# Kernel optimization log

Hardware: AMD Instinct MI355X
Metric: run time of the kernel (lower is better)

Reference implementation:

```python
import jax, jax.numpy as jnp
import numpy as np

N_NODES = 50000
N_EDGES = 800000
IN_DIM = 256
NHID = 64
OUT_DIM = 64
DEPTH = 4
P = 2.0


def _gcn_conv(x, W, b, src, dst, n):
    # PyG GCNConv: xW, add self-loops, sym-normalize, aggregate src->dst, + bias
    xw = x @ W
    loop = jnp.arange(n)
    s = jnp.concatenate([src, loop])
    d = jnp.concatenate([dst, loop])
    deg = jax.ops.segment_sum(jnp.ones_like(d, dtype=xw.dtype), d, num_segments=n)
    dis = jnp.where(deg > 0, jax.lax.rsqrt(jnp.maximum(deg, 1.0)), 0.0)
    w = dis[s] * dis[d]  # [E+n]
    out = jax.ops.segment_sum(w[:, None] * xw[s], d, num_segments=n)
    return out + b


def _g2_gate(x, W, b, src, dst, n):
    xg = jax.nn.relu(_gcn_conv(x, W, b, src, dst, n))
    diff = jnp.abs(xg[src] - xg[dst]) ** P  # [E, nhid]
    sums = jax.ops.segment_sum(diff, src, num_segments=n)
    cnt = jax.ops.segment_sum(jnp.ones((src.shape[0],), dtype=x.dtype), src, num_segments=n)
    return jnp.tanh(sums / jnp.maximum(cnt, 1.0)[:, None])


def setup_inputs() -> dict:
    key = jax.random.key(0)
    ks = jax.random.split(key, 10)
    x = jax.random.normal(ks[0], (N_NODES, IN_DIM), dtype=jnp.float32)
    edge_index = jax.random.randint(ks[1], (2, N_EDGES), 0, N_NODES, dtype=jnp.int64 if jax.config.jax_enable_x64 else jnp.int32)
    s = 0.05
    return {
        "x": x,
        "edge_index": edge_index,
        "enc_w": jax.random.normal(ks[2], (IN_DIM, NHID), dtype=jnp.float32) * s,
        "enc_b": jnp.zeros((NHID,), dtype=jnp.float32),
        "conv_w": jax.random.normal(ks[3], (NHID, NHID), dtype=jnp.float32) * s,
        "conv_b": jnp.zeros((NHID,), dtype=jnp.float32),
        "gg_w": jax.random.normal(ks[4], (NHID, NHID), dtype=jnp.float32) * s,
        "gg_b": jnp.zeros((NHID,), dtype=jnp.float32),
        "dec_w": jax.random.normal(ks[5], (NHID, OUT_DIM), dtype=jnp.float32) * s,
        "dec_b": jnp.zeros((OUT_DIM,), dtype=jnp.float32),
    }


def reference(x, edge_index, enc_w, enc_b, conv_w, conv_b, gg_w, gg_b, dec_w, dec_b):
    n = x.shape[0]
    src, dst = edge_index[0], edge_index[1]
    # eval mode: dropouts are identity
    X = jax.nn.relu(x @ enc_w + enc_b)
    for _ in range(DEPTH):
        X_ = jax.nn.relu(_gcn_conv(X, conv_w, conv_b, src, dst, n))
        tau = _g2_gate(X, gg_w, gg_b, src, dst, n)
        X = (1.0 - tau) * X + tau * X_
    X = jax.nn.relu(X @ dec_w + dec_b)
    return X
```

## Files before the change

kernel.cpp:

```cpp
#include <hip/hip_runtime.h>
#include <math.h>

#define NN 50000
#define NE 800000
#define IND 256
#define NH 64
#define DEPTH 4
#define PART_DIV 6250


__device__ __forceinline__ unsigned short f2bf(float f) {
    unsigned int x = __float_as_uint(f);
    unsigned int r = (x + 0x7fffu + ((x >> 16) & 1u)) >> 16;
    return (unsigned short)r;
}
__device__ __forceinline__ unsigned int pack2bf(float lo, float hi) {
    return (unsigned int)f2bf(lo) | ((unsigned int)f2bf(hi) << 16);
}
__device__ __forceinline__ ushort4 f4_to_us4(float4 f) {
    ushort4 u;
    u.x = f2bf(f.x); u.y = f2bf(f.y); u.z = f2bf(f.z); u.w = f2bf(f.w);
    return u;
}
__device__ __forceinline__ void acc8(float* a, uint4 r) {
    a[0] += __uint_as_float(r.x << 16); a[1] += __uint_as_float(r.x & 0xffff0000u);
    a[2] += __uint_as_float(r.y << 16); a[3] += __uint_as_float(r.y & 0xffff0000u);
    a[4] += __uint_as_float(r.z << 16); a[5] += __uint_as_float(r.z & 0xffff0000u);
    a[6] += __uint_as_float(r.w << 16); a[7] += __uint_as_float(r.w & 0xffff0000u);
}
__device__ __forceinline__ void unpack8(float* a, uint4 r) {
    a[0] = __uint_as_float(r.x << 16); a[1] = __uint_as_float(r.x & 0xffff0000u);
    a[2] = __uint_as_float(r.y << 16); a[3] = __uint_as_float(r.y & 0xffff0000u);
    a[4] = __uint_as_float(r.z << 16); a[5] = __uint_as_float(r.z & 0xffff0000u);
    a[6] = __uint_as_float(r.w << 16); a[7] = __uint_as_float(r.w & 0xffff0000u);
}
__device__ __forceinline__ void accd8(float* a, const float* xg, uint4 r) {
    float e;
    e = xg[0] - __uint_as_float(r.x << 16);         a[0] += e * e;
    e = xg[1] - __uint_as_float(r.x & 0xffff0000u); a[1] += e * e;
    e = xg[2] - __uint_as_float(r.y << 16);         a[2] += e * e;
    e = xg[3] - __uint_as_float(r.y & 0xffff0000u); a[3] += e * e;
    e = xg[4] - __uint_as_float(r.z << 16);         a[4] += e * e;
    e = xg[5] - __uint_as_float(r.z & 0xffff0000u); a[5] += e * e;
    e = xg[6] - __uint_as_float(r.w << 16);         a[6] += e * e;
    e = xg[7] - __uint_as_float(r.w & 0xffff0000u); a[7] += e * e;
}
__device__ __forceinline__ float tanh_pos(float x) {
    float t = __expf(-2.f * x);
    return (1.f - t) / (1.f + t);
}


__global__ void count_deg(const int* __restrict__ src, const int* __restrict__ dst,
                          int* __restrict__ degin, int* __restrict__ degout) {
    int e = blockIdx.x * blockDim.x + threadIdx.x;
    if (e < NE) {
        atomicAdd(&degout[src[e]], 1);
        atomicAdd(&degin[dst[e]], 1);
    }
}

__global__ void scan2(const int* __restrict__ in0, int* __restrict__ out0,
                      const int* __restrict__ in1, int* __restrict__ out1, int n) {
    __shared__ int sums[1024];
    const int* in = blockIdx.x ? in1 : in0;
    int* out = blockIdx.x ? out1 : out0;
    int t = threadIdx.x;
    int chunk = (n + 1023) / 1024;
    int lo = t * chunk;
    int hi = lo + chunk; if (hi > n) hi = n;
    int s = 0;
    for (int i = lo; i < hi; ++i) s += in[i];
    sums[t] = s;
    __syncthreads();
    for (int off = 1; off < 1024; off <<= 1) {
        int v = (t >= off) ? sums[t - off] : 0;
        __syncthreads();
        sums[t] += v;
        __syncthreads();
    }
    int run = (t == 0) ? 0 : sums[t - 1];
    for (int i = lo; i < hi; ++i) { out[i] = run; run += in[i]; }
    if (t == 0) out[n] = sums[1023];
}

__global__ void init_node(const int* __restrict__ degin, const int* __restrict__ degout,
                          const int* __restrict__ off_dst, const int* __restrict__ off_src,
                          int* __restrict__ cur_dst, int* __restrict__ cur_src,
                          float* __restrict__ dis, float* __restrict__ cntf) {
    int i = blockIdx.x * blockDim.x + threadIdx.x;
    if (i < NN) {
        dis[i] = rsqrtf((float)(degin[i] + 1));
        int od = degout[i];
        cntf[i] = (float)(od > 0 ? od : 1);
        cur_dst[i] = off_dst[i];
        cur_src[i] = off_src[i];
    }
}

__global__ void fill_csr_part(const int* __restrict__ src, const int* __restrict__ dst,
                              int* __restrict__ cur_dst, int* __restrict__ cur_src,
                              int* __restrict__ srcs_by_dst, int* __restrict__ dsts_by_src,
                              int nGroups) {
    int p = blockIdx.x & 7;
    int g = blockIdx.x >> 3;
    for (int e = g * 256 + threadIdx.x; e < NE; e += nGroups * 256) {
        int s = src[e], d = dst[e];
        if (d / PART_DIV == p) {
            int pos = atomicAdd(&cur_dst[d], 1);
            srcs_by_dst[pos] = s;
        }
        if (s / PART_DIV == p) {
            int pos = atomicAdd(&cur_src[s], 1);
            dsts_by_src[pos] = d;
        }
    }
}

template<int K, bool RELU, bool WSC>
__global__ __launch_bounds__(256) void gemm64b(const float* __restrict__ X,
                                               const float* __restrict__ W,
                                               const float* __restrict__ bias,
                                               const float* __restrict__ rowscale,
                                               float* __restrict__ out,
                                               unsigned short* __restrict__ xsc, int n) {
    __shared__ float Ws[64 * 64];
    __shared__ float Xs[64][68];
    int tid = threadIdx.x;
    int row0 = blockIdx.x * 64;
    int r16 = tid >> 4;
    int cg = tid & 15;
    float4 acc[4];
#pragma unroll
    for (int t = 0; t < 4; ++t) acc[t] = make_float4(0.f, 0.f, 0.f, 0.f);

    for (int kc = 0; kc < K; kc += 64) {
        const float4* W4 = (const float4*)(W + (size_t)kc * 64);
        float4* Ws4 = (float4*)Ws;
#pragma unroll
        for (int t = 0; t < 4; ++t) Ws4[tid + t * 256] = W4[tid + t * 256];
#pragma unroll
        for (int t = 0; t < 4; ++t) {
            int r = r16 + t * 16;
            int grow = row0 + r;
            float4 xv = make_float4(0.f, 0.f, 0.f, 0.f);
            if (grow < n) xv = *(const float4*)(X + (size_t)grow * K + kc + cg * 4);
            Xs[r][cg * 4 + 0] = xv.x; Xs[r][cg * 4 + 1] = xv.y;
            Xs[r][cg * 4 + 2] = xv.z; Xs[r][cg * 4 + 3] = xv.w;
        }
        __syncthreads();
#pragma unroll
        for (int k = 0; k < 64; ++k) {
            float4 w4 = ((const float4*)Ws)[k * 16 + cg];
#pragma unroll
            for (int t = 0; t < 4; ++t) {
                float xv = Xs[r16 + t * 16][k];
                acc[t].x += xv * w4.x; acc[t].y += xv * w4.y;
                acc[t].z += xv * w4.z; acc[t].w += xv * w4.w;
            }
        }
        __syncthreads();
    }

    float4 b4 = ((const float4*)bias)[cg];
#pragma unroll
    for (int t = 0; t < 4; ++t) {
        int row = row0 + r16 + t * 16;
        if (row < n) {
            float4 o;
            o.x = acc[t].x + b4.x; o.y = acc[t].y + b4.y;
            o.z = acc[t].z + b4.z; o.w = acc[t].w + b4.w;
            if (RELU) {
                o.x = fmaxf(o.x, 0.f); o.y = fmaxf(o.y, 0.f);
                o.z = fmaxf(o.z, 0.f); o.w = fmaxf(o.w, 0.f);
            }
            ((float4*)(out + (size_t)row * 64))[cg] = o;
            if (WSC) {
                float s = rowscale[row];
                float4 o2 = make_float4(o.x * s, o.y * s, o.z * s, o.w * s);
                ((ushort4*)(xsc + (size_t)row * 64))[cg] = f4_to_us4(o2);
            }
        }
    }
}

template<bool OUTBF>
__global__ __launch_bounds__(256) void gemm64z(const float* __restrict__ Z,
                                               const float* __restrict__ W,
                                               const float* __restrict__ bias,
                                               float* __restrict__ outf,
                                               unsigned short* __restrict__ outb, int n) {
    __shared__ float Ws[64 * 64];
    __shared__ float Xs[64][68];
    int tid = threadIdx.x;
    int row0 = blockIdx.x * 64;
    int r16 = tid >> 4;
    int cg = tid & 15;
    float4 acc[4];
#pragma unroll
    for (int t = 0; t < 4; ++t) acc[t] = make_float4(0.f, 0.f, 0.f, 0.f);

    {
        const float4* W4 = (const float4*)W;
        float4* Ws4 = (float4*)Ws;
#pragma unroll
        for (int t = 0; t < 4; ++t) Ws4[tid + t * 256] = W4[tid + t * 256];
#pragma unroll
        for (int t = 0; t < 4; ++t) {
            int r = r16 + t * 16;
            int grow = row0 + r;
            float4 xv = make_float4(0.f, 0.f, 0.f, 0.f);
            if (grow < n) xv = *(const float4*)(Z + (size_t)grow * 64 + cg * 4);
            Xs[r][cg * 4 + 0] = xv.x; Xs[r][cg * 4 + 1] = xv.y;
            Xs[r][cg * 4 + 2] = xv.z; Xs[r][cg * 4 + 3] = xv.w;
        }
        __syncthreads();
#pragma unroll
        for (int k = 0; k < 64; ++k) {
            float4 w4 = ((const float4*)Ws)[k * 16 + cg];
#pragma unroll
            for (int t = 0; t < 4; ++t) {
                float xv = Xs[r16 + t * 16][k];
                acc[t].x += xv * w4.x; acc[t].y += xv * w4.y;
                acc[t].z += xv * w4.z; acc[t].w += xv * w4.w;
            }
        }
    }

    float4 b4 = ((const float4*)bias)[cg];
#pragma unroll
    for (int t = 0; t < 4; ++t) {
        int row = row0 + r16 + t * 16;
        if (row < n) {
            float4 o;
            o.x = fmaxf(acc[t].x + b4.x, 0.f); o.y = fmaxf(acc[t].y + b4.y, 0.f);
            o.z = fmaxf(acc[t].z + b4.z, 0.f); o.w = fmaxf(acc[t].w + b4.w, 0.f);
            if (OUTBF) {
                ((ushort4*)(outb + (size_t)row * 64))[cg] = f4_to_us4(o);
            } else {
                ((float4*)(outf + (size_t)row * 64))[cg] = o;
            }
        }
    }
}

__global__ __launch_bounds__(256) void zgather(
    const unsigned short* __restrict__ Xbf,
    const int* __restrict__ off, const int* __restrict__ nbr,
    const float* __restrict__ dis, float* __restrict__ Z)
{
    int t = blockIdx.x * 256 + threadIdx.x;
    int node = t >> 3, l8 = t & 7;
    if (node >= NN) return;
    const uint4* Xb = (const uint4*)Xbf;
    float a[8];
    unpack8(a, Xb[(size_t)node * 8 + l8]);
    int lo = off[node], hi = off[node + 1];
    int j = lo;
    for (; j + 3 < hi; j += 4) {
        int s0 = nbr[j], s1 = nbr[j + 1], s2 = nbr[j + 2], s3 = nbr[j + 3];
        uint4 r0 = Xb[(size_t)s0 * 8 + l8];
        uint4 r1 = Xb[(size_t)s1 * 8 + l8];
        uint4 r2 = Xb[(size_t)s2 * 8 + l8];
        uint4 r3 = Xb[(size_t)s3 * 8 + l8];
        acc8(a, r0); acc8(a, r1); acc8(a, r2); acc8(a, r3);
    }
    for (; j < hi; ++j) {
        acc8(a, Xb[(size_t)nbr[j] * 8 + l8]);
    }
    float di = dis[node];
    float* zp = Z + (size_t)node * 64 + l8 * 8;
    *(float4*)(zp)     = make_float4(di * a[0], di * a[1], di * a[2], di * a[3]);
    *(float4*)(zp + 4) = make_float4(di * a[4], di * a[5], di * a[6], di * a[7]);
}

__global__ __launch_bounds__(256) void gate_update8(
    const unsigned short* __restrict__ Cbf, const float* __restrict__ Xn,
    float* __restrict__ X, unsigned short* __restrict__ Xbf,
    const int* __restrict__ off, const int* __restrict__ nbr,
    const float* __restrict__ cntf, const float* __restrict__ dis)
{
    int t = blockIdx.x * 256 + threadIdx.x;
    int node = t >> 3, l8 = t & 7;
    if (node >= NN) return;
    const uint4* Cb = (const uint4*)Cbf;
    float xg[8];
    unpack8(xg, Cb[(size_t)node * 8 + l8]);
    float a[8] = {0.f, 0.f, 0.f, 0.f, 0.f, 0.f, 0.f, 0.f};
    int lo = off[node], hi = off[node + 1];
    int j = lo;
    for (; j + 3 < hi; j += 4) {
        int d0 = nbr[j], d1 = nbr[j + 1], d2 = nbr[j + 2], d3 = nbr[j + 3];
        uint4 r0 = Cb[(size_t)d0 * 8 + l8];
        uint4 r1 = Cb[(size_t)d1 * 8 + l8];
        uint4 r2 = Cb[(size_t)d2 * 8 + l8];
        uint4 r3 = Cb[(size_t)d3 * 8 + l8];
        accd8(a, xg, r0); accd8(a, xg, r1); accd8(a, xg, r2); accd8(a, xg, r3);
    }
    for (; j < hi; ++j) {
        accd8(a, xg, Cb[(size_t)nbr[j] * 8 + l8]);
    }
    float inv = 1.f / cntf[node];
    float di = dis[node];
    const float* xop = X + (size_t)node * 64 + l8 * 8;
    const float* xnp = Xn + (size_t)node * 64 + l8 * 8;
    float o[8];
#pragma unroll
    for (int k = 0; k < 8; ++k) {
        float tau = tanh_pos(a[k] * inv);
        float xo = xop[k], xn = xnp[k];
        o[k] = xo + tau * (xn - xo);
    }
    float* xp = X + (size_t)node * 64 + l8 * 8;
    *(float4*)(xp)     = make_float4(o[0], o[1], o[2], o[3]);
    *(float4*)(xp + 4) = make_float4(o[4], o[5], o[6], o[7]);
    uint4 pk;
    pk.x = pack2bf(o[0] * di, o[1] * di);
    pk.y = pack2bf(o[2] * di, o[3] * di);
    pk.z = pack2bf(o[4] * di, o[5] * di);
    pk.w = pack2bf(o[6] * di, o[7] * di);
    ((uint4*)Xbf)[(size_t)node * 8 + l8] = pk;
}


extern "C" void kernel_launch(void* const* d_in, const int* in_sizes, int n_in,
                              void* d_out, int out_size, void* d_ws, size_t ws_size,
                              hipStream_t stream) {
    const float* x      = (const float*)d_in[0];
    const int*   ei     = (const int*)d_in[1];
    const float* enc_w  = (const float*)d_in[2];
    const float* enc_b  = (const float*)d_in[3];
    const float* conv_w = (const float*)d_in[4];
    const float* conv_b = (const float*)d_in[5];
    const float* gg_w   = (const float*)d_in[6];
    const float* gg_b   = (const float*)d_in[7];
    const float* dec_w  = (const float*)d_in[8];
    const float* dec_b  = (const float*)d_in[9];
    float* out = (float*)d_out;

    const int* src = ei;
    const int* dst = ei + NE;

    char* p = (char*)d_ws;
    auto alloc = [&](size_t bytes) -> void* {
        void* r = (void*)p;
        p += (bytes + 255) & ~(size_t)255;
        return r;
    };
    float* X   = (float*)alloc((size_t)NN * 64 * 4);
    float* Zb  = (float*)alloc((size_t)NN * 64 * 4);
    float* B   = (float*)alloc((size_t)NN * 64 * 4);
    unsigned short* Xbf = (unsigned short*)alloc((size_t)NN * 64 * 2);
    unsigned short* Cbf = (unsigned short*)alloc((size_t)NN * 64 * 2);
    float* dis  = (float*)alloc((size_t)NN * 4);
    float* cntf = (float*)alloc((size_t)NN * 4);
    int* degin   = (int*)alloc((size_t)NN * 4);
    int* degout  = (int*)alloc((size_t)NN * 4);
    int* off_dst = (int*)alloc((size_t)(NN + 1) * 4);
    int* off_src = (int*)alloc((size_t)(NN + 1) * 4);
    int* cur_dst = (int*)alloc((size_t)NN * 4);
    int* cur_src = (int*)alloc((size_t)NN * 4);
    int* sbd     = (int*)alloc((size_t)NE * 4);
    int* dbs     = (int*)alloc((size_t)NE * 4);

    hipMemsetAsync(degin, 0, (size_t)NN * 4, stream);
    hipMemsetAsync(degout, 0, (size_t)NN * 4, stream);

    const int EB = (NE + 255) / 256;
    const int NB = (NN + 255) / 256;
    count_deg<<<EB, 256, 0, stream>>>(src, dst, degin, degout);
    scan2<<<2, 1024, 0, stream>>>(degin, off_dst, degout, off_src, NN);
    init_node<<<NB, 256, 0, stream>>>(degin, degout, off_dst, off_src,
                                      cur_dst, cur_src, dis, cntf);
    const int NGROUPS = 104;
    fill_csr_part<<<8 * NGROUPS, 256, 0, stream>>>(src, dst, cur_dst, cur_src,
                                                   sbd, dbs, NGROUPS);

    const int GB = (NN + 63) / 64;
    const int OB = ((NN * 8) + 255) / 256;

    gemm64b<IND, true, true><<<GB, 256, 0, stream>>>(x, enc_w, enc_b, dis, X, Xbf, NN);

    for (int l = 0; l < DEPTH; ++l) {
        zgather<<<OB, 256, 0, stream>>>(Xbf, off_dst, sbd, dis, Zb);
        gemm64z<false><<<GB, 256, 0, stream>>>(Zb, conv_w, conv_b, B, nullptr, NN);
        gemm64z<true><<<GB, 256, 0, stream>>>(Zb, gg_w, gg_b, nullptr, Cbf, NN);
        gate_update8<<<OB, 256, 0, stream>>>(Cbf, B, X, Xbf, off_src, dbs, cntf, dis);
    }

    gemm64b<NH, true, false><<<GB, 256, 0, stream>>>(X, dec_w, dec_b, nullptr, out, nullptr, NN);
}
```

Measured before the change: 764.7 us.

## Parallelize degree scan across blocks and partition degree counting by node range

Replaces the single-block-per-array 1024-thread serial-chunk scan with a three-phase multi-block scan (wave shuffles, per-block sums, add-back), so the prefix sum uses many CUs instead of two. Degree counting now uses a partitioned grid where each of 8 block groups only performs atomics for nodes in its range, the same scheme fill_csr_part already uses, to keep atomics local. The cost is two extra launches, a temporary buffer, and every partition group re-reading the full edge list.

```diff
diff --git a/kernel.cpp b/kernel.cpp
--- a/kernel.cpp
+++ b/kernel.cpp
@@ -7,6 +7,7 @@
 #define NH 64
 #define DEPTH 4
 #define PART_DIV 6250
+#define SB 49
 
 
 __device__ __forceinline__ unsigned short f2bf(float f) {
@@ -51,37 +52,83 @@
 }
 
 
-__global__ void count_deg(const int* __restrict__ src, const int* __restrict__ dst,
-                          int* __restrict__ degin, int* __restrict__ degout) {
-    int e = blockIdx.x * blockDim.x + threadIdx.x;
-    if (e < NE) {
-        atomicAdd(&degout[src[e]], 1);
-        atomicAdd(&degin[dst[e]], 1);
-    }
-}
-
-__global__ void scan2(const int* __restrict__ in0, int* __restrict__ out0,
-                      const int* __restrict__ in1, int* __restrict__ out1, int n) {
-    __shared__ int sums[1024];
-    const int* in = blockIdx.x ? in1 : in0;
-    int* out = blockIdx.x ? out1 : out0;
+__global__ void count_deg_part(const int* __restrict__ src, const int* __restrict__ dst,
+                               int* __restrict__ degin, int* __restrict__ degout,
+                               int nGroups) {
+    int p = blockIdx.x & 7;
+    int g = blockIdx.x >> 3;
+    for (int e = g * 256 + threadIdx.x; e < NE; e += nGroups * 256) {
+        int s = src[e], d = dst[e];
+        if (d / PART_DIV == p) atomicAdd(&degin[d], 1);
+        if (s / PART_DIV == p) atomicAdd(&degout[s], 1);
+    }
+}
+
+__global__ __launch_bounds__(512) void scan_p1(const int* __restrict__ in0,
+                                               const int* __restrict__ in1,
+                                               int* __restrict__ tmp,
+                                               int* __restrict__ bsum) {
+    int a = blockIdx.x / SB;
+    int b = blockIdx.x % SB;
+    const int* in = a ? in1 : in0;
     int t = threadIdx.x;
-    int chunk = (n + 1023) / 1024;
-    int lo = t * chunk;
-    int hi = lo + chunk; if (hi > n) hi = n;
-    int s = 0;
-    for (int i = lo; i < hi; ++i) s += in[i];
-    sums[t] = s;
+    int base = b * 1024 + t * 2;
+    int v0 = (base < NN) ? in[base] : 0;
+    int v1 = (base + 1 < NN) ? in[base + 1] : 0;
+    int v = v0 + v1;
+    int x = v;
+#pragma unroll
+    for (int off = 1; off < 64; off <<= 1) {
+        int u = __shfl_up(x, off);
+        if ((t & 63) >= off) x += u;
+    }
+    __shared__ int ws[8];
+    int wid = t >> 6, lane = t & 63;
+    if (lane == 63) ws[wid] = x;
     __syncthreads();
-    for (int off = 1; off < 1024; off <<= 1) {
-        int v = (t >= off) ? sums[t - off] : 0;
-        __syncthreads();
-        sums[t] += v;
-        __syncthreads();
-    }
-    int run = (t == 0) ? 0 : sums[t - 1];
-    for (int i = lo; i < hi; ++i) { out[i] = run; run += in[i]; }
-    if (t == 0) out[n] = sums[1023];
+    if (t == 0) {
+        int run = 0;
+#pragma unroll
+        for (int w = 0; w < 8; ++w) { int s = ws[w]; ws[w] = run; run += s; }
+    }
+    __syncthreads();
+    x += ws[wid];
+    int excl = x - v;
+    if (base < NN) tmp[a * NN + base] = excl;
+    if (base + 1 < NN) tmp[a * NN + base + 1] = excl + v0;
+    if (t == 511) bsum[a * SB + b] = x;
+}
+
+__global__ __launch_bounds__(128) void scan_p2(int* __restrict__ bsum,
+                                               int* __restrict__ out0,
+                                               int* __restrict__ out1) {
+    int t = threadIdx.x;
+    int a = t >> 6, lane = t & 63;
+    int v = (lane < SB) ? bsum[a * SB + lane] : 0;
+    int x = v;
+#pragma unroll
+    for (int off = 1; off < 64; off <<= 1) {
+        int u = __shfl_up(x, off);
+        if (lane >= off) x += u;
+    }
+    if (lane < SB) bsum[a * SB + lane] = x - v;
+    if (lane == SB - 1) {
+        if (a == 0) out0[NN] = x; else out1[NN] = x;
+    }
+}
+
+__global__ __launch_bounds__(512) void scan_p3(const int* __restrict__ tmp,
+                                               const int* __restrict__ bsum,
+                                               int* __restrict__ out0,
+                                               int* __restrict__ out1) {
+    int a = blockIdx.x / SB;
+    int b = blockIdx.x % SB;
+    int* out = a ? out1 : out0;
+    int add = bsum[a * SB + b];
+    int t = threadIdx.x;
+    int base = b * 1024 + t * 2;
+    if (base < NN) out[base] = tmp[a * NN + base] + add;
+    if (base + 1 < NN) out[base + 1] = tmp[a * NN + base + 1] + add;
 }
 
 __global__ void init_node(const int* __restrict__ degin, const int* __restrict__ degout,
@@ -208,9 +255,11 @@
 #pragma unroll
         for (int t = 0; t < 4; ++t) {
             int r = r16 + t * 16;
-            int grow = row0 + r;
+            int grow = row0 + t * 16 + r16;
+            (void)grow;
+            int gr = row0 + r;
             float4 xv = make_float4(0.f, 0.f, 0.f, 0.f);
-            if (grow < n) xv = *(const float4*)(Z + (size_t)grow * 64 + cg * 4);
+            if (gr < n) xv = *(const float4*)(Z + (size_t)gr * 64 + cg * 4);
             Xs[r][cg * 4 + 0] = xv.x; Xs[r][cg * 4 + 1] = xv.y;
             Xs[r][cg * 4 + 2] = xv.z; Xs[r][cg * 4 + 3] = xv.w;
         }
@@ -362,17 +411,20 @@
     int* cur_src = (int*)alloc((size_t)NN * 4);
     int* sbd     = (int*)alloc((size_t)NE * 4);
     int* dbs     = (int*)alloc((size_t)NE * 4);
+    int* stmp    = (int*)alloc((size_t)2 * NN * 4);
+    int* bsum    = (int*)alloc((size_t)2 * SB * 4);
 
     hipMemsetAsync(degin, 0, (size_t)NN * 4, stream);
     hipMemsetAsync(degout, 0, (size_t)NN * 4, stream);
 
-    const int EB = (NE + 255) / 256;
     const int NB = (NN + 255) / 256;
-    count_deg<<<EB, 256, 0, stream>>>(src, dst, degin, degout);
-    scan2<<<2, 1024, 0, stream>>>(degin, off_dst, degout, off_src, NN);
+    const int NGROUPS = 104;
+    count_deg_part<<<8 * NGROUPS, 256, 0, stream>>>(src, dst, degin, degout, NGROUPS);
+    scan_p1<<<2 * SB, 512, 0, stream>>>(degin, degout, stmp, bsum);
+    scan_p2<<<1, 128, 0, stream>>>(bsum, off_dst, off_src);
+    scan_p3<<<2 * SB, 512, 0, stream>>>(stmp, bsum, off_dst, off_src);
     init_node<<<NB, 256, 0, stream>>>(degin, degout, off_dst, off_src,
                                       cur_dst, cur_src, dis, cntf);
-    const int NGROUPS = 104;
     fill_csr_part<<<8 * NGROUPS, 256, 0, stream>>>(src, dst, cur_dst, cur_src,
                                                    sbd, dbs, NGROUPS);
 
```

Result: faster. 697.1 us (-8.8%).
